# Performance work log

Measured on AMD Instinct MI355X. Metric: run time of the kernel, lower is better.

## Reference

```python
import jax, jax.numpy as jnp
import numpy as np

EPS = 1e-5
ABIT = 8
WBIT = 8


def ste_round(x):
    # straight-through rounding (HAWQ SymmetricQuantFunction)
    return x + jax.lax.stop_gradient(jnp.round(x) - x)


def quant_act(x, bit=ABIT):
    # per-tensor symmetric activation quantization (QuantAct)
    n = 2.0 ** (bit - 1) - 1  # 127
    scale = jnp.max(jnp.abs(x)) / n
    x_int = jnp.clip(ste_round(x / scale), -n - 1, n)
    return x_int * scale, scale


def setup_inputs() -> dict:
    key = jax.random.key(0)
    k = jax.random.split(key, 6)
    B, C_in, H, W, C_out = 32, 512, 32, 32, 128
    x = jax.random.normal(k[0], (B, C_in, H, W), jnp.float32)
    # incoming activation scale (input assumed already 8-bit quantized)
    act_scaling_factor = (jnp.max(jnp.abs(x)) / 127.0).reshape(1)
    bn_gamma = jax.random.uniform(k[1], (C_in,), jnp.float32, 0.5, 1.5)
    bn_beta = jax.random.normal(k[2], (C_in,), jnp.float32) * 0.1
    bn_mean = jax.random.normal(k[3], (C_in,), jnp.float32) * 0.1
    bn_var = jax.random.uniform(k[4], (C_in,), jnp.float32, 0.5, 1.5)
    conv_weight = jax.random.normal(k[5], (C_out, C_in, 3, 3), jnp.float32) / np.sqrt(C_in * 9)
    return {"x": x, "act_scaling_factor": act_scaling_factor,
            "bn_gamma": bn_gamma, "bn_beta": bn_beta,
            "bn_mean": bn_mean, "bn_var": bn_var,
            "conv_weight": conv_weight}


def reference(x, act_scaling_factor, bn_gamma, bn_beta, bn_mean, bn_var, conv_weight):
    nw = 2.0 ** (WBIT - 1) - 1  # 127
    s_in = act_scaling_factor.reshape(())

    # ---- QuantBn: fold BN into per-channel affine, quantize weight/bias ----
    w_bn = bn_gamma / jnp.sqrt(bn_var + EPS)            # [C_in]
    b_bn = bn_beta - bn_mean * w_bn                      # [C_in]
    ws_bn = jnp.max(jnp.abs(w_bn)) / nw                  # per-tensor weight scale
    w_int = jnp.clip(ste_round(w_bn / ws_bn), -nw - 1, nw)
    bn_sf = ws_bn * s_in                                 # bn output scaling factor
    b_int = ste_round(b_bn / bn_sf)
    x_int = x / s_in
    x = (x_int * w_int[None, :, None, None] + b_int[None, :, None, None]) * bn_sf

    # ---- ReLU ----
    x = jax.nn.relu(x)

    # ---- QuantAct: requantize activations to 8 bit ----
    x, s_act = quant_act(x)

    # ---- QuantConv2d: per-output-channel 8-bit weight quant, int conv ----
    ws_c = jnp.max(jnp.abs(conv_weight), axis=(1, 2, 3)) / nw       # [C_out]
    w_cint = jnp.clip(ste_round(conv_weight / ws_c[:, None, None, None]), -nw - 1, nw)
    y_int = jax.lax.conv_general_dilated(
        x / s_act, w_cint, window_strides=(1, 1), padding=((1, 1), (1, 1)),
        dimension_numbers=("NCHW", "OIHW", "NCHW"))
    conv_sf = s_act * ws_c                               # [C_out]
    y = y_int * conv_sf[None, :, None, None]

    # ---- QuantAct output requant ----
    y, s_out = quant_act(y)
    return (y, s_out)
```

## Files before the change

### kernel.cpp

```cpp
#include <hip/hip_runtime.h>


typedef int v4i __attribute__((ext_vector_type(4)));

#define WS_A1    64
#define WS_B1    2112
#define WS_WSC   4160
#define WS_XMX   4672
#define WS_XMN   6720
#define WS_WQ    8768
#define WS_X2    598592
#define WS_ZROW  18424384

__device__ __forceinline__ float wave_max(float m) {
#pragma unroll
    for (int off = 32; off; off >>= 1) m = fmaxf(m, __shfl_xor(m, off));
    return m;
}

__device__ __forceinline__ void stage16(const char* g, char* s, int lane) {
#if defined(__has_builtin) && __has_builtin(__builtin_amdgcn_global_load_lds)
    __builtin_amdgcn_global_load_lds(
        (const __attribute__((address_space(1))) void*)g,
        (__attribute__((address_space(3))) void*)s, 16, 0, 0);
#else
    *(v4i*)(s + lane * 16) = *(const v4i*)g;
#endif
}

__global__ __launch_bounds__(512) void k_prep(
    const float* __restrict__ gamma, const float* __restrict__ beta,
    const float* __restrict__ mean,  const float* __restrict__ var,
    const float* __restrict__ asf,   const float* __restrict__ cw,
    const float4* __restrict__ x4,
    float* ws_f, unsigned* ws_u, float* __restrict__ wsc,
    signed char* __restrict__ wq) {
    int t = threadIdx.x;
    int bid = blockIdx.x;
    __shared__ float red[16];
    if (bid < 512) {
        int c = bid;
        float mx = -3.4e38f, mn = 3.4e38f;
#pragma unroll
        for (int r = 0; r < 16; ++r) {
            int bbb = r * 2 + (t >> 8);
            float4 v = x4[((size_t)(bbb * 512 + c)) * 256 + (t & 255)];
            mx = fmaxf(mx, fmaxf(fmaxf(v.x, v.y), fmaxf(v.z, v.w)));
            mn = fminf(mn, fminf(fminf(v.x, v.y), fminf(v.z, v.w)));
        }
        mx = wave_max(mx);
        mn = -wave_max(-mn);
        if ((t & 63) == 0) { red[t >> 6] = mx; red[8 + (t >> 6)] = mn; }
        __syncthreads();
        if (t == 0) {
            float M = red[0], N = red[8];
#pragma unroll
            for (int i = 1; i < 8; ++i) { M = fmaxf(M, red[i]); N = fminf(N, red[8 + i]); }
            ws_f[WS_XMX / 4 + c] = M;
            ws_f[WS_XMN / 4 + c] = N;
        }
    } else if (bid < 640) {
        int co = bid - 512;
        const float* w = cw + (size_t)co * 4608;
        float m = 0.f;
        for (int j = t; j < 4608; j += 512) m = fmaxf(m, fabsf(w[j]));
        m = wave_max(m);
        if ((t & 63) == 0) red[t >> 6] = m;
        __syncthreads();
        float mall = red[0];
#pragma unroll
        for (int i = 1; i < 8; ++i) mall = fmaxf(mall, red[i]);
        float sc = mall / 127.0f;
        if (t == 0) wsc[co] = sc;
        int ci = t >> 6, cq = (t >> 4) & 3, cb = t & 15;
#pragma unroll
        for (int tap = 0; tap < 9; ++tap) {
            float q = fminf(fmaxf(rintf(w[t * 9 + tap] / sc), -128.f), 127.f);
            wq[(((size_t)(tap * 8 + ci) * 4 + cq) * 128 + co) * 16 + cb] = (signed char)q;
        }
    } else {
        float wbn = gamma[t] / sqrtf(var[t] + 1e-5f);
        float bbn = beta[t] - mean[t] * wbn;
        float m = wave_max(fabsf(wbn));
        if ((t & 63) == 0) red[t >> 6] = m;
        __syncthreads();
        float mall = red[0];
#pragma unroll
        for (int i = 1; i < 8; ++i) mall = fmaxf(mall, red[i]);
        float ws_bn = mall / 127.0f;
        float s_in  = asf[0];
        float bn_sf = ws_bn * s_in;
        float wint  = fminf(fmaxf(rintf(wbn / ws_bn), -128.f), 127.f);
        float bint  = rintf(bbn / bn_sf);
        ws_f[WS_A1 / 4 + t] = wint * bn_sf / s_in;
        ws_f[WS_B1 / 4 + t] = bint * bn_sf;
        if (t == 0) ws_u[1] = 0u;
    }
}

__global__ __launch_bounds__(256) void k_xquant(
    const float4* __restrict__ x4, float* __restrict__ ws_f,
    unsigned* __restrict__ x2u, unsigned* __restrict__ zrowu) {
    int bb = 31 - (blockIdx.x >> 5), h = blockIdx.x & 31;
    const float* A1 = ws_f + WS_A1 / 4;
    const float* B1 = ws_f + WS_B1 / 4;
    const float* XMX = ws_f + WS_XMX / 4;
    const float* XMN = ws_f + WS_XMN / 4;
    int t = threadIdx.x;

    __shared__ float sred[4];
    float cand = 0.f;
#pragma unroll
    for (int c0 = 0; c0 < 512; c0 += 256) {
        int c = c0 + t;
        float A = A1[c], B = B1[c];
        cand = fmaxf(cand, fmaxf(fmaf(XMX[c], A, B), fmaf(XMN[c], A, B)));
    }
    cand = wave_max(cand);
    if ((t & 63) == 0) sred[t >> 6] = cand;
    __syncthreads();
    float xm = fmaxf(fmaxf(sred[0], sred[1]), fmaxf(sred[2], sred[3]));
    float inv_sact = 127.0f / xm;
    if (blockIdx.x == 0 && t == 0) ws_f[3] = xm / 127.0f;

    size_t rowd = (size_t)(bb * 32 + h) * 4352;
    {
        int p = t >> 3, side = (t >> 2) & 1, d = t & 3;
        x2u[rowd + (p * 34 + side * 33) * 4 + d] = 0u;
    }
    if (blockIdx.x < 17) {
        int idx = blockIdx.x * 256 + t;
        if (idx < 4352) zrowu[idx] = 0u;
    }

    __shared__ unsigned lds[512 * 9];

#pragma unroll
    for (int it = 0; it < 16; ++it) {
        int idx = it * 256 + t;
        int c = idx >> 3, f4 = idx & 7;
        float4 v = x4[((size_t)bb * 512 + c) * 256 + h * 8 + f4];
        float A = A1[c] * inv_sact, B = B1[c] * inv_sact;
        unsigned q0 = (unsigned)(int)fminf(rintf(fmaxf(fmaf(v.x, A, B), 0.f)), 127.f);
        unsigned q1 = (unsigned)(int)fminf(rintf(fmaxf(fmaf(v.y, A, B), 0.f)), 127.f);
        unsigned q2 = (unsigned)(int)fminf(rintf(fmaxf(fmaf(v.z, A, B), 0.f)), 127.f);
        unsigned q3 = (unsigned)(int)fminf(rintf(fmaxf(fmaf(v.w, A, B), 0.f)), 127.f);
        lds[c * 9 + f4] = q0 | (q1 << 8) | (q2 << 16) | (q3 << 24);
    }
    __syncthreads();

#pragma unroll
    for (int it = 0; it < 4; ++it) {
        int p = it * 8 + (t >> 5);
        int s = (t >> 2) & 7;
        int k = t & 3;
        unsigned L[16];
#pragma unroll
        for (int j = 0; j < 16; ++j) L[j] = lds[(p * 16 + j) * 9 + s];
        uint4 o;
        unsigned* op = (unsigned*)&o;
#pragma unroll
        for (int d = 0; d < 4; ++d)
            op[d] = ((L[4 * d] >> (8 * k)) & 255u) |
                    (((L[4 * d + 1] >> (8 * k)) & 255u) << 8) |
                    (((L[4 * d + 2] >> (8 * k)) & 255u) << 16) |
                    (((L[4 * d + 3] >> (8 * k)) & 255u) << 24);
        *(uint4*)(x2u + rowd + (size_t)(p * 34 + s * 4 + 1 + k) * 4) = o;
    }
}

__global__ __launch_bounds__(256, 2) void k_conv(
    const unsigned char* __restrict__ x2, const unsigned char* __restrict__ zrow,
    const signed char* __restrict__ wq,
    const float* __restrict__ wsc, const float* __restrict__ ws_f,
    unsigned* __restrict__ amaxy, float* __restrict__ y) {
    __shared__ char ldsb[73728];
    int t = threadIdx.x;
    int lane = t & 63, wv = t >> 6;
    int kv = wv & 1, rp = wv >> 1;
    int m = lane & 15, quad = lane >> 4;

    int bid = blockIdx.x;
    int tile = (bid & 7) * 64 + (bid >> 3);
    int ch = tile & 1;
    int rg = (tile >> 1) & 7;
    int bb = tile >> 4;
    int co0 = ch * 64;
    int h0 = rg * 4 + rp * 2;

    const unsigned char* xb = x2 + (size_t)bb * (32 * 17408);
    const v4i* rpt[4];
#pragma unroll
    for (int j = 0; j < 4; ++j) {
        int row = h0 - 1 + j;
        rpt[j] = (const v4i*)(((unsigned)row < 32u) ? (xb + (size_t)row * 17408) : zrow);
    }

    v4i acc[4][4];
#pragma unroll
    for (int i = 0; i < 4; ++i)
#pragma unroll
        for (int j = 0; j < 4; ++j) acc[i][j] = (v4i){0, 0, 0, 0};

    int abase = quad * 34 + m;

    for (int j = 0; j < 4; ++j) {
#pragma unroll
        for (int i = 0; i < 18; ++i) {
            int c = wv * 18 + i;
            int kvs = (c >= 36) ? 1 : 0;
            int rem = c - kvs * 36;
            int tap = rem >> 2, cq = rem & 3;
            int ci = kvs * 4 + j;
            const char* g = (const char*)wq +
                ((((size_t)(tap * 8 + ci) * 4 + cq) * 128 + co0) * 16) + lane * 16;
            char* s = ldsb + (((kvs * 9 + tap) * 4 + cq) << 10);
            stage16(g, s, lane);
        }
        __syncthreads();

        int ci = kv * 4 + j;
        const v4i* bbase = (const v4i*)ldsb + kv * 2304;
#pragma unroll
        for (int kh = 0; kh < 3; ++kh)
#pragma unroll
            for (int kw = 0; kw < 3; ++kw) {
                int tap = kh * 3 + kw;
                v4i a[4];
#pragma unroll
                for (int mt = 0; mt < 4; ++mt)
                    a[mt] = rpt[kh + (mt >> 1)][ci * 136 + abase + kw + (mt & 1) * 16];
#pragma unroll
                for (int nt = 0; nt < 4; ++nt) {
                    v4i bf = bbase[(tap * 4 + quad) * 64 + nt * 16 + m];
#pragma unroll
                    for (int mt = 0; mt < 4; ++mt)
                        acc[mt][nt] = __builtin_amdgcn_mfma_i32_16x16x64_i8(a[mt], bf, acc[mt][nt], 0, 0, 0);
                }
            }
        __syncthreads();
    }

    v4i* red = (v4i*)ldsb;
    if (kv == 1) {
#pragma unroll
        for (int mt = 0; mt < 4; ++mt)
#pragma unroll
            for (int nt = 0; nt < 4; ++nt)
                red[((rp * 16 + mt * 4 + nt) << 6) + lane] = acc[mt][nt];
    }
    __syncthreads();
    if (kv == 0) {
#pragma unroll
        for (int mt = 0; mt < 4; ++mt)
#pragma unroll
            for (int nt = 0; nt < 4; ++nt) {
                v4i p = red[((rp * 16 + mt * 4 + nt) << 6) + lane];
                acc[mt][nt].x += p.x; acc[mt][nt].y += p.y;
                acc[mt][nt].z += p.z; acc[mt][nt].w += p.w;
            }

        float s_act = ws_f[3];
        float mx = 0.f;
#pragma unroll
        for (int nt = 0; nt < 4; ++nt) {
            int co = co0 + nt * 16 + m;
            float sf = s_act * wsc[co];
#pragma unroll
            for (int mt = 0; mt < 4; ++mt) {
                int row = h0 + (mt >> 1);
                float* yb = y + ((size_t)(bb * 128 + co)) * 1024 + row * 32 + (mt & 1) * 16;
                float4 vv;
                vv.x = (float)acc[mt][nt][0] * sf;
                vv.y = (float)acc[mt][nt][1] * sf;
                vv.z = (float)acc[mt][nt][2] * sf;
                vv.w = (float)acc[mt][nt][3] * sf;
                *(float4*)(yb + quad * 4) = vv;
                mx = fmaxf(mx, fmaxf(fmaxf(fabsf(vv.x), fabsf(vv.y)),
                                     fmaxf(fabsf(vv.z), fabsf(vv.w))));
            }
        }
        mx = wave_max(mx);
        if (lane == 0) atomicMax(amaxy, __float_as_uint(mx));
    }
}

__global__ __launch_bounds__(256) void k_yquant(float* __restrict__ yout,
                                                const unsigned* __restrict__ ws_u) {
    float s_out = __uint_as_float(ws_u[1]) / 127.0f;
    float4* y4 = (float4*)yout;
    int stride = gridDim.x * blockDim.x;
    for (int i = blockIdx.x * blockDim.x + threadIdx.x; i < 1048576; i += stride) {
        float4 v = y4[i];
        v.x = fminf(fmaxf(rintf(v.x / s_out), -128.f), 127.f) * s_out;
        v.y = fminf(fmaxf(rintf(v.y / s_out), -128.f), 127.f) * s_out;
        v.z = fminf(fmaxf(rintf(v.z / s_out), -128.f), 127.f) * s_out;
        v.w = fminf(fmaxf(rintf(v.w / s_out), -128.f), 127.f) * s_out;
        y4[i] = v;
    }
    if (blockIdx.x == 0 && threadIdx.x == 0) yout[4194304] = s_out;
}

extern "C" void kernel_launch(void* const* d_in, const int* in_sizes, int n_in,
                              void* d_out, int out_size, void* d_ws, size_t ws_size,
                              hipStream_t stream) {
    const float* x     = (const float*)d_in[0];
    const float* asf   = (const float*)d_in[1];
    const float* gamma = (const float*)d_in[2];
    const float* beta  = (const float*)d_in[3];
    const float* mean  = (const float*)d_in[4];
    const float* var   = (const float*)d_in[5];
    const float* cw    = (const float*)d_in[6];

    float*    ws_f = (float*)d_ws;
    unsigned* ws_u = (unsigned*)d_ws;
    signed char*   wq   = (signed char*)d_ws + WS_WQ;
    unsigned char* x2   = (unsigned char*)d_ws + WS_X2;
    unsigned char* zrow = (unsigned char*)d_ws + WS_ZROW;
    float* y = (float*)d_out;

    k_prep<<<641, 512, 0, stream>>>(gamma, beta, mean, var, asf, cw,
                                    (const float4*)x, ws_f, ws_u,
                                    ws_f + WS_WSC / 4, wq);
    k_xquant<<<1024, 256, 0, stream>>>((const float4*)x, ws_f,
                                       (unsigned*)x2, (unsigned*)zrow);
    k_conv<<<512, 256, 0, stream>>>(x2, zrow, wq, ws_f + WS_WSC / 4,
                                    ws_f, ws_u + 1, y);
    k_yquant<<<1024, 256, 0, stream>>>(y, ws_u);
}
```

Before: 159.9 us.

## Fuse output requantization into conv kernel via grid-wide barrier

Removes the separate y requantization kernel. The conv blocks compute the absolute max of their accumulators before storing, publish it with an atomic max, and then synchronize through a global atomic counter barrier. After the barrier each block quantizes its results in registers and writes y only once. This avoids re-reading and rewriting the full output tensor, but it relies on all 512 blocks being resident at the same time and adds spin-wait cost.

```diff
diff --git a/kernel.cpp b/kernel.cpp
--- a/kernel.cpp
+++ b/kernel.cpp
@@ -94,7 +94,7 @@
         float bint  = rintf(bbn / bn_sf);
         ws_f[WS_A1 / 4 + t] = wint * bn_sf / s_in;
         ws_f[WS_B1 / 4 + t] = bint * bn_sf;
-        if (t == 0) ws_u[1] = 0u;
+        if (t == 0) { ws_u[1] = 0u; ws_u[2] = 0u; }
     }
 }
 
@@ -173,7 +173,7 @@
     const unsigned char* __restrict__ x2, const unsigned char* __restrict__ zrow,
     const signed char* __restrict__ wq,
     const float* __restrict__ wsc, const float* __restrict__ ws_f,
-    unsigned* __restrict__ amaxy, float* __restrict__ y) {
+    unsigned* __restrict__ ws_u, float* __restrict__ y) {
     __shared__ char ldsb[73728];
     int t = threadIdx.x;
     int lane = t & 63, wv = t >> 6;
@@ -250,18 +250,40 @@
                 red[((rp * 16 + mt * 4 + nt) << 6) + lane] = acc[mt][nt];
     }
     __syncthreads();
+
+    float s_act = ws_f[3];
     if (kv == 0) {
-#pragma unroll
-        for (int mt = 0; mt < 4; ++mt)
-#pragma unroll
-            for (int nt = 0; nt < 4; ++nt) {
+        float mx = 0.f;
+#pragma unroll
+        for (int nt = 0; nt < 4; ++nt) {
+            float sf = s_act * wsc[co0 + nt * 16 + m];
+#pragma unroll
+            for (int mt = 0; mt < 4; ++mt) {
                 v4i p = red[((rp * 16 + mt * 4 + nt) << 6) + lane];
                 acc[mt][nt].x += p.x; acc[mt][nt].y += p.y;
                 acc[mt][nt].z += p.z; acc[mt][nt].w += p.w;
+                mx = fmaxf(mx, fmaxf(
+                    fmaxf(fabsf((float)acc[mt][nt].x * sf), fabsf((float)acc[mt][nt].y * sf)),
+                    fmaxf(fabsf((float)acc[mt][nt].z * sf), fabsf((float)acc[mt][nt].w * sf))));
             }
-
-        float s_act = ws_f[3];
-        float mx = 0.f;
+        }
+        mx = wave_max(mx);
+        if (lane == 0) atomicMax(ws_u + 1, __float_as_uint(mx));
+    }
+
+    __syncthreads();
+    if (t == 0) {
+        __hip_atomic_fetch_add(ws_u + 2, 1u, __ATOMIC_ACQ_REL, __HIP_MEMORY_SCOPE_AGENT);
+        int guard = 0;
+        while (__hip_atomic_load(ws_u + 2, __ATOMIC_ACQUIRE, __HIP_MEMORY_SCOPE_AGENT) < 512u
+               && ++guard < (1 << 24))
+            __builtin_amdgcn_s_sleep(2);
+    }
+    __syncthreads();
+
+    if (kv == 0) {
+        float s_out = __uint_as_float(
+            __hip_atomic_load(ws_u + 1, __ATOMIC_ACQUIRE, __HIP_MEMORY_SCOPE_AGENT)) / 127.0f;
 #pragma unroll
         for (int nt = 0; nt < 4; ++nt) {
             int co = co0 + nt * 16 + m;
@@ -275,30 +297,15 @@
                 vv.y = (float)acc[mt][nt][1] * sf;
                 vv.z = (float)acc[mt][nt][2] * sf;
                 vv.w = (float)acc[mt][nt][3] * sf;
+                vv.x = fminf(fmaxf(rintf(vv.x / s_out), -128.f), 127.f) * s_out;
+                vv.y = fminf(fmaxf(rintf(vv.y / s_out), -128.f), 127.f) * s_out;
+                vv.z = fminf(fmaxf(rintf(vv.z / s_out), -128.f), 127.f) * s_out;
+                vv.w = fminf(fmaxf(rintf(vv.w / s_out), -128.f), 127.f) * s_out;
                 *(float4*)(yb + quad * 4) = vv;
-                mx = fmaxf(mx, fmaxf(fmaxf(fabsf(vv.x), fabsf(vv.y)),
-                                     fmaxf(fabsf(vv.z), fabsf(vv.w))));
             }
         }
-        mx = wave_max(mx);
-        if (lane == 0) atomicMax(amaxy, __float_as_uint(mx));
-    }
-}
-
-__global__ __launch_bounds__(256) void k_yquant(float* __restrict__ yout,
-                                                const unsigned* __restrict__ ws_u) {
-    float s_out = __uint_as_float(ws_u[1]) / 127.0f;
-    float4* y4 = (float4*)yout;
-    int stride = gridDim.x * blockDim.x;
-    for (int i = blockIdx.x * blockDim.x + threadIdx.x; i < 1048576; i += stride) {
-        float4 v = y4[i];
-        v.x = fminf(fmaxf(rintf(v.x / s_out), -128.f), 127.f) * s_out;
-        v.y = fminf(fmaxf(rintf(v.y / s_out), -128.f), 127.f) * s_out;
-        v.z = fminf(fmaxf(rintf(v.z / s_out), -128.f), 127.f) * s_out;
-        v.w = fminf(fmaxf(rintf(v.w / s_out), -128.f), 127.f) * s_out;
-        y4[i] = v;
-    }
-    if (blockIdx.x == 0 && threadIdx.x == 0) yout[4194304] = s_out;
+        if (blockIdx.x == 0 && t == 0) y[4194304] = s_out;
+    }
 }
 
 extern "C" void kernel_launch(void* const* d_in, const int* in_sizes, int n_in,
@@ -325,6 +332,5 @@
     k_xquant<<<1024, 256, 0, stream>>>((const float4*)x, ws_f,
                                        (unsigned*)x2, (unsigned*)zrow);
     k_conv<<<512, 256, 0, stream>>>(x2, zrow, wq, ws_f + WS_WSC / 4,
-                                    ws_f, ws_u + 1, y);
-    k_yquant<<<1024, 256, 0, stream>>>(y, ws_u);
-}
+                                    ws_f, ws_u, y);
+}
```

Measured after the change: 259.8 us. +62.5%, slower.

## Split conv tile across waves by output channel instead of K, drop LDS reduction

Applied to the files above, without the earlier changes.

The conv kernel now uses smaller tiles: each block covers 2 output rows and 64 channels. Each wave owns one row and 32 channels and runs the full K loop over all 8 input-channel groups, instead of splitting K across waves and reducing partial sums through LDS. This halves the LDS buffer and the accumulator count, raises the occupancy target to 4 blocks per CU, and doubles the grid. In exchange, weights are staged per input-channel group with twice as many barriers, and each block reuses each staged weight tile over fewer activation rows.

```diff
diff --git a/kernel.cpp b/kernel.cpp
--- a/kernel.cpp
+++ b/kernel.cpp
@@ -169,24 +169,24 @@
     }
 }
 
-__global__ __launch_bounds__(256, 2) void k_conv(
+__global__ __launch_bounds__(256, 4) void k_conv(
     const unsigned char* __restrict__ x2, const unsigned char* __restrict__ zrow,
     const signed char* __restrict__ wq,
     const float* __restrict__ wsc, const float* __restrict__ ws_f,
     unsigned* __restrict__ amaxy, float* __restrict__ y) {
-    __shared__ char ldsb[73728];
+    __shared__ char ldsb[36864];
     int t = threadIdx.x;
     int lane = t & 63, wv = t >> 6;
-    int kv = wv & 1, rp = wv >> 1;
+    int nh = wv & 1, wr = wv >> 1;
     int m = lane & 15, quad = lane >> 4;
 
     int bid = blockIdx.x;
-    int tile = (bid & 7) * 64 + (bid >> 3);
+    int tile = (bid & 7) * 128 + (bid >> 3);
     int ch = tile & 1;
-    int rg = (tile >> 1) & 7;
-    int bb = tile >> 4;
+    int rg = (tile >> 1) & 15;
+    int bb = tile >> 5;
     int co0 = ch * 64;
-    int h0 = rg * 4 + rp * 2;
+    int h0 = rg * 2;
 
     const unsigned char* xb = x2 + (size_t)bb * (32 * 17408);
     const v4i* rpt[4];
@@ -196,92 +196,71 @@
         rpt[j] = (const v4i*)(((unsigned)row < 32u) ? (xb + (size_t)row * 17408) : zrow);
     }
 
-    v4i acc[4][4];
-#pragma unroll
-    for (int i = 0; i < 4; ++i)
-#pragma unroll
-        for (int j = 0; j < 4; ++j) acc[i][j] = (v4i){0, 0, 0, 0};
+    v4i acc[2][2];
+#pragma unroll
+    for (int i = 0; i < 2; ++i)
+#pragma unroll
+        for (int j = 0; j < 2; ++j) acc[i][j] = (v4i){0, 0, 0, 0};
 
     int abase = quad * 34 + m;
-
-    for (int j = 0; j < 4; ++j) {
-#pragma unroll
-        for (int i = 0; i < 18; ++i) {
-            int c = wv * 18 + i;
-            int kvs = (c >= 36) ? 1 : 0;
-            int rem = c - kvs * 36;
-            int tap = rem >> 2, cq = rem & 3;
-            int ci = kvs * 4 + j;
+    const v4i* bv = (const v4i*)ldsb;
+
+    for (int ci = 0; ci < 8; ++ci) {
+        __syncthreads();
+#pragma unroll
+        for (int i = 0; i < 9; ++i) {
+            int c = wv * 9 + i;
+            int tap = c >> 2, cq = c & 3;
             const char* g = (const char*)wq +
                 ((((size_t)(tap * 8 + ci) * 4 + cq) * 128 + co0) * 16) + lane * 16;
-            char* s = ldsb + (((kvs * 9 + tap) * 4 + cq) << 10);
-            stage16(g, s, lane);
-        }
-        __syncthreads();
-
-        int ci = kv * 4 + j;
-        const v4i* bbase = (const v4i*)ldsb + kv * 2304;
+            stage16(g, ldsb + (c << 10), lane);
+        }
+        __syncthreads();
+
 #pragma unroll
         for (int kh = 0; kh < 3; ++kh)
 #pragma unroll
             for (int kw = 0; kw < 3; ++kw) {
                 int tap = kh * 3 + kw;
-                v4i a[4];
-#pragma unroll
-                for (int mt = 0; mt < 4; ++mt)
-                    a[mt] = rpt[kh + (mt >> 1)][ci * 136 + abase + kw + (mt & 1) * 16];
-#pragma unroll
-                for (int nt = 0; nt < 4; ++nt) {
-                    v4i bf = bbase[(tap * 4 + quad) * 64 + nt * 16 + m];
-#pragma unroll
-                    for (int mt = 0; mt < 4; ++mt)
-                        acc[mt][nt] = __builtin_amdgcn_mfma_i32_16x16x64_i8(a[mt], bf, acc[mt][nt], 0, 0, 0);
+                v4i a0 = rpt[wr + kh][ci * 136 + abase + kw];
+                v4i a1 = rpt[wr + kh][ci * 136 + abase + kw + 16];
+#pragma unroll
+                for (int nt = 0; nt < 2; ++nt) {
+                    v4i bf = bv[(tap * 4 + quad) * 64 + nh * 32 + nt * 16 + m];
+                    acc[0][nt] = __builtin_amdgcn_mfma_i32_16x16x64_i8(a0, bf, acc[0][nt], 0, 0, 0);
+                    acc[1][nt] = __builtin_amdgcn_mfma_i32_16x16x64_i8(a1, bf, acc[1][nt], 0, 0, 0);
                 }
             }
-        __syncthreads();
-    }
-
-    v4i* red = (v4i*)ldsb;
-    if (kv == 1) {
-#pragma unroll
-        for (int mt = 0; mt < 4; ++mt)
-#pragma unroll
-            for (int nt = 0; nt < 4; ++nt)
-                red[((rp * 16 + mt * 4 + nt) << 6) + lane] = acc[mt][nt];
-    }
+    }
+
+    float s_act = ws_f[3];
+    float mx = 0.f;
+    int row = h0 + wr;
+#pragma unroll
+    for (int nt = 0; nt < 2; ++nt) {
+        int co = co0 + nh * 32 + nt * 16 + m;
+        float sf = s_act * wsc[co];
+        float* yb = y + ((size_t)(bb * 128 + co)) * 1024 + row * 32;
+#pragma unroll
+        for (int mt = 0; mt < 2; ++mt) {
+            float4 vv;
+            vv.x = (float)acc[mt][nt][0] * sf;
+            vv.y = (float)acc[mt][nt][1] * sf;
+            vv.z = (float)acc[mt][nt][2] * sf;
+            vv.w = (float)acc[mt][nt][3] * sf;
+            *(float4*)(yb + mt * 16 + quad * 4) = vv;
+            mx = fmaxf(mx, fmaxf(fmaxf(fabsf(vv.x), fabsf(vv.y)),
+                                 fmaxf(fabsf(vv.z), fabsf(vv.w))));
+        }
+    }
+    mx = wave_max(mx);
     __syncthreads();
-    if (kv == 0) {
-#pragma unroll
-        for (int mt = 0; mt < 4; ++mt)
-#pragma unroll
-            for (int nt = 0; nt < 4; ++nt) {
-                v4i p = red[((rp * 16 + mt * 4 + nt) << 6) + lane];
-                acc[mt][nt].x += p.x; acc[mt][nt].y += p.y;
-                acc[mt][nt].z += p.z; acc[mt][nt].w += p.w;
-            }
-
-        float s_act = ws_f[3];
-        float mx = 0.f;
-#pragma unroll
-        for (int nt = 0; nt < 4; ++nt) {
-            int co = co0 + nt * 16 + m;
-            float sf = s_act * wsc[co];
-#pragma unroll
-            for (int mt = 0; mt < 4; ++mt) {
-                int row = h0 + (mt >> 1);
-                float* yb = y + ((size_t)(bb * 128 + co)) * 1024 + row * 32 + (mt & 1) * 16;
-                float4 vv;
-                vv.x = (float)acc[mt][nt][0] * sf;
-                vv.y = (float)acc[mt][nt][1] * sf;
-                vv.z = (float)acc[mt][nt][2] * sf;
-                vv.w = (float)acc[mt][nt][3] * sf;
-                *(float4*)(yb + quad * 4) = vv;
-                mx = fmaxf(mx, fmaxf(fmaxf(fabsf(vv.x), fabsf(vv.y)),
-                                     fmaxf(fabsf(vv.z), fabsf(vv.w))));
-            }
-        }
-        mx = wave_max(mx);
-        if (lane == 0) atomicMax(amaxy, __float_as_uint(mx));
+    if (lane == 0) ((float*)ldsb)[wv] = mx;
+    __syncthreads();
+    if (t == 0) {
+        float* r = (float*)ldsb;
+        float M = fmaxf(fmaxf(r[0], r[1]), fmaxf(r[2], r[3]));
+        atomicMax(amaxy, __float_as_uint(M));
     }
 }
 
@@ -324,7 +303,7 @@
                                     ws_f + WS_WSC / 4, wq);
     k_xquant<<<1024, 256, 0, stream>>>((const float4*)x, ws_f,
                                        (unsigned*)x2, (unsigned*)zrow);
-    k_conv<<<512, 256, 0, stream>>>(x2, zrow, wq, ws_f + WS_WSC / 4,
-                                    ws_f, ws_u + 1, y);
+    k_conv<<<1024, 256, 0, stream>>>(x2, zrow, wq, ws_f + WS_WSC / 4,
+                                     ws_f, ws_u + 1, y);
     k_yquant<<<1024, 256, 0, stream>>>(y, ws_u);
 }
```

After: 167.2 us. 4.6% more time.
